# Kernel tuning notes

Hardware: AMD Instinct MI355X
Metric: run time of the kernel (lower is better)

Reference implementation:

```python
import jax, jax.numpy as jnp
import numpy as np

B = 2; QD = 128; H = QD; W = QD; NQ = QD * QD
EMBED = 256; HEADS = 8; POINTS = 4; D = EMBED // HEADS; FFN = 512


def setup_inputs() -> dict:
    key = jax.random.key(0)
    ks = jax.random.split(key, 16)
    s = 0.02
    rn = lambda k, shp: jax.random.normal(k, shp, jnp.float32) * s
    return {
        'q': jax.random.normal(ks[0], (B, NQ, EMBED), jnp.float32),
        'W_off': rn(ks[1], (EMBED, HEADS * POINTS * 2)),
        'b_off': rn(ks[2], (HEADS * POINTS * 2,)),
        'W_attn': rn(ks[3], (EMBED, HEADS * POINTS)),
        'b_attn': rn(ks[4], (HEADS * POINTS,)),
        'W_val': rn(ks[5], (EMBED, EMBED)),
        'b_val': rn(ks[6], (EMBED,)),
        'W_out': rn(ks[7], (EMBED, EMBED)),
        'b_out': rn(ks[8], (EMBED,)),
        'W1': rn(ks[9], (EMBED, FFN)),
        'b1': rn(ks[10], (FFN,)),
        'W2': rn(ks[11], (FFN, EMBED)),
        'b2': rn(ks[12], (EMBED,)),
        'gamma': jnp.ones((EMBED,), jnp.float32),
        'beta': jnp.zeros((EMBED,), jnp.float32),
    }


def _layernorm(x, g, b):
    m = x.mean(-1, keepdims=True)
    v = ((x - m) ** 2).mean(-1, keepdims=True)
    return (x - m) * jax.lax.rsqrt(v + 1e-5) * g + b


def _msda(q, W_off, b_off, W_attn, b_attn, W_val, b_val, W_out, b_out):
    # value projection; value == query here. (B, NQ, EMBED)
    value = q @ W_val + b_val
    v = value.reshape(B, NQ, HEADS, D).transpose(0, 2, 1, 3)  # (B, heads, Nv, D)

    off = (q @ W_off + b_off).reshape(B, NQ, HEADS, POINTS, 2)
    aw = jax.nn.softmax((q @ W_attn + b_attn).reshape(B, NQ, HEADS, POINTS), axis=-1)

    # reference points: torch.meshgrid(linspace, linspace, indexing='xy')
    lin = jnp.linspace(0.0, 1.0, QD)
    gx, gy = jnp.meshgrid(lin, lin, indexing='xy')
    ref = jnp.stack([gx, gy], -1).reshape(1, NQ, 1, 1, 2)

    # offset_normalizer = [W, H]; sampling locations in [0,1]
    loc = ref + off / jnp.array([W, H], jnp.float32)
    # grid_sample bilinear, align_corners=False: pixel = loc * size - 0.5
    px = (loc[..., 0] * W - 0.5).transpose(0, 2, 1, 3)  # (B, heads, NQ, P)
    py = (loc[..., 1] * H - 0.5).transpose(0, 2, 1, 3)

    x0 = jnp.floor(px)
    y0 = jnp.floor(py)
    sampled = jnp.zeros((B, HEADS, NQ, POINTS, D), jnp.float32)
    for dy in (0.0, 1.0):
        for dx in (0.0, 1.0):
            xi = x0 + dx
            yi = y0 + dy
            wgt = (1.0 - jnp.abs(px - xi)) * (1.0 - jnp.abs(py - yi))
            valid = ((xi >= 0) & (xi <= W - 1) & (yi >= 0) & (yi <= H - 1)).astype(jnp.float32)
            idx = (jnp.clip(yi, 0, H - 1).astype(jnp.int32) * W
                   + jnp.clip(xi, 0, W - 1).astype(jnp.int32))  # (B, heads, NQ, P)
            g = jnp.take_along_axis(v, idx.reshape(B, HEADS, NQ * POINTS, 1), axis=2)
            g = g.reshape(B, HEADS, NQ, POINTS, D)
            sampled = sampled + g * (wgt * valid)[..., None]

    awt = aw.transpose(0, 2, 1, 3)  # (B, heads, NQ, P)
    out = (sampled * awt[..., None]).sum(3)  # (B, heads, NQ, D)
    out = out.transpose(0, 2, 1, 3).reshape(B, NQ, EMBED)
    # mmcv: dropout(output_proj(out)) + identity ; dropout is identity at eval
    return out @ W_out + b_out + q


def reference(q, W_off, b_off, W_attn, b_attn, W_val, b_val, W_out, b_out,
              W1, b1, W2, b2, gamma, beta):
    attn = _msda(q, W_off, b_off, W_attn, b_attn, W_val, b_val, W_out, b_out)
    x = attn + q  # outer residual in the module (in addition to mmcv's internal one)
    ffn = _layernorm(jax.nn.relu(x @ W1 + b1) @ W2 + b2, gamma, beta)
    return x + ffn
```

## Files before the change

### kernel.cpp

```cpp
#include <hip/hip_runtime.h>
#include <hip/hip_bf16.h>
#include <cstddef>
#include <cstdint>

#define B_      2
#define QD_     128
#define NQ_     (QD_ * QD_)
#define EMBED_  256
#define HEADS_  8
#define POINTS_ 4
#define FFN_    512
#define RTOT_   (B_ * NQ_)
#define NCATP_  384

using bf16x8 = __attribute__((ext_vector_type(8))) short;
using f32x4  = __attribute__((ext_vector_type(4))) float;

__device__ __forceinline__ short f2bf(float f) {
    unsigned u = __float_as_uint(f);
    u += 0x7FFFu + ((u >> 16) & 1u);
    return (short)(u >> 16);
}
__device__ __forceinline__ float bf2f(short s) {
    return __uint_as_float(((unsigned)(unsigned short)s) << 16);
}

#define GLDS(gp, lp) __builtin_amdgcn_global_load_lds( \
        (const __attribute__((address_space(1))) void*)(gp), \
        (__attribute__((address_space(3))) void*)(lp), 16, 0, 0)

#define WCAT_ELEMS  (NCATP_ * 256)
#define WOUT_ELEMS  (256 * 256)
#define W1_ELEMS    (512 * 256)
#define W2_ELEMS    (256 * 512)
#define PREP_TOTAL  (WCAT_ELEMS + WOUT_ELEMS + W1_ELEMS + W2_ELEMS)
#define CVT_BLOCKS  (RTOT_ * EMBED_ / 8 / 256)
#define PREP_BLOCKS ((PREP_TOTAL + 255) / 256)

__global__ __launch_bounds__(256) void prep_all(
        const float* __restrict__ q, short* __restrict__ qbf,
        const float* __restrict__ Wv, const float* __restrict__ Wo,
        const float* __restrict__ Wa, const float* __restrict__ bv,
        const float* __restrict__ bo, const float* __restrict__ ba,
        const float* __restrict__ W_out, const float* __restrict__ W1,
        const float* __restrict__ W2,
        short* __restrict__ WcatT, short* __restrict__ WoutT,
        short* __restrict__ W1T, short* __restrict__ W2T,
        float* __restrict__ bcat) {
    const int b = blockIdx.x;
    if (b < CVT_BLOCKS) {
        const size_t i = (size_t)b * 256 + threadIdx.x;
        const float4 f0 = *(const float4*)(q + i * 8);
        const float4 f1 = *(const float4*)(q + i * 8 + 4);
        bf16x8 v;
        v[0] = f2bf(f0.x); v[1] = f2bf(f0.y); v[2] = f2bf(f0.z); v[3] = f2bf(f0.w);
        v[4] = f2bf(f1.x); v[5] = f2bf(f1.y); v[6] = f2bf(f1.z); v[7] = f2bf(f1.w);
        *(bf16x8*)(qbf + i * 8) = v;
        return;
    }
    int idx = (b - CVT_BLOCKS) * 256 + threadIdx.x;
    if (idx < WCAT_ELEMS) {
        int c = idx >> 8, k = idx & 255;
        float v = 0.f;
        if (c < 256)      v = Wv[k * 256 + c];
        else if (c < 320) v = Wo[k * 64 + (c - 256)];
        else if (c < 352) v = Wa[k * 32 + (c - 320)];
        WcatT[idx] = f2bf(v);
    } else if (idx < WCAT_ELEMS + WOUT_ELEMS) {
        int j = idx - WCAT_ELEMS; int c = j >> 8, k = j & 255;
        WoutT[j] = f2bf(W_out[k * 256 + c]);
    } else if (idx < WCAT_ELEMS + WOUT_ELEMS + W1_ELEMS) {
        int j = idx - (WCAT_ELEMS + WOUT_ELEMS); int c = j >> 8, k = j & 255;
        W1T[j] = f2bf(W1[k * 512 + c]);
    } else if (idx < PREP_TOTAL) {
        int j = idx - (WCAT_ELEMS + WOUT_ELEMS + W1_ELEMS); int c = j >> 9, k = j & 511;
        W2T[j] = f2bf(W2[k * 256 + c]);
    }
    if (idx < NCATP_) {
        float v = 0.f;
        if (idx < 256)      v = bv[idx];
        else if (idx < 320) v = bo[idx - 256];
        else if (idx < 352) v = ba[idx - 320];
        bcat[idx] = v;
    }
}

enum { EP_RELU_BF16 = 1, EP_ADD2Q_BF16 = 2, EP_SPLIT = 3 };

template <int EP>
__global__ __launch_bounds__(256) void gemm_mfma(
        const short* __restrict__ A,
        const short* __restrict__ Bt,
        const float* __restrict__ bias,
        const short* __restrict__ extra,
        float* __restrict__ Cf,
        short* __restrict__ Cb,
        int M, int N, int K) {
    __shared__ __align__(16) short As[2][128 * 64];
    __shared__ __align__(16) short Bs[2][128 * 64];

    const int t    = threadIdx.x;
    const int ln   = t & 63;
    const int w    = t >> 6;
    const int wr   = w >> 1;
    const int wc   = w & 1;
    const int lrow = ln & 15;
    const int lkg  = ln >> 4;

    const int gx   = gridDim.x;
    const int nwg  = gx * gridDim.y;
    const int flat = blockIdx.y * gx + blockIdx.x;
    const int q8   = nwg >> 3;
    const int swz  = (flat & 7) * q8 + (flat >> 3);
    const int row0 = (swz / gx) * 128;
    const int col0 = (swz % gx) * 128;

    f32x4 acc[4][4] = {};

    auto stage = [&](int buf, int k0) {
        #pragma unroll
        for (int j = 0; j < 4; ++j) {
            const int c0 = (w * 4 + j) * 64;
            const int c  = c0 + ln;
            const int r  = c >> 3;
            const int s  = (c & 7) ^ (r & 7);
            GLDS(A  + (size_t)(row0 + r) * K + (k0 + s * 8), &As[buf][c0 * 8]);
            GLDS(Bt + (size_t)(col0 + r) * K + (k0 + s * 8), &Bs[buf][c0 * 8]);
        }
    };

    stage(0, 0);
    __syncthreads();
    int cur = 0;
    for (int k0 = 0; k0 < K; k0 += 64) {
        if (k0 + 64 < K) stage(cur ^ 1, k0 + 64);
        #pragma unroll
        for (int ks = 0; ks < 2; ++ks) {
            const int slot = ((ks * 4 + lkg) ^ (lrow & 7)) * 8;
            bf16x8 af[4], bfr[4];
            #pragma unroll
            for (int m = 0; m < 4; ++m)
                af[m] = *(const bf16x8*)&As[cur][(wr * 64 + m * 16 + lrow) * 64 + slot];
            #pragma unroll
            for (int n = 0; n < 4; ++n)
                bfr[n] = *(const bf16x8*)&Bs[cur][(wc * 64 + n * 16 + lrow) * 64 + slot];
            #pragma unroll
            for (int m = 0; m < 4; ++m)
                #pragma unroll
                for (int n = 0; n < 4; ++n)
                    acc[m][n] = __builtin_amdgcn_mfma_f32_16x16x32_bf16(
                        af[m], bfr[n], acc[m][n], 0, 0, 0);
        }
        __syncthreads();
        cur ^= 1;
    }

    const int orow = (ln >> 4) * 4;
    const int ocol = ln & 15;
    #pragma unroll
    for (int m = 0; m < 4; ++m) {
        #pragma unroll
        for (int n = 0; n < 4; ++n) {
            const int col = col0 + wc * 64 + n * 16 + ocol;
            const float bv = bias[col];
            #pragma unroll
            for (int rr = 0; rr < 4; ++rr) {
                const int row = row0 + wr * 64 + m * 16 + orow + rr;
                float v = acc[m][n][rr] + bv;
                if (EP == EP_SPLIT) {
                    if (col < 256) Cb[(size_t)row * 256 + col] = f2bf(v);
                    else           Cf[(size_t)row * 128 + (col - 256)] = v;
                } else if (EP == EP_RELU_BF16) {
                    Cb[(size_t)row * N + col] = f2bf(fmaxf(v, 0.f));
                } else if (EP == EP_ADD2Q_BF16) {
                    v += 2.f * bf2f(extra[(size_t)row * N + col]);
                    Cb[(size_t)row * N + col] = f2bf(v);
                }
            }
        }
    }
}

__global__ __launch_bounds__(256) void gemm_ln(
        const short* __restrict__ A,
        const short* __restrict__ Bt,
        const float* __restrict__ bias,
        const short* __restrict__ xres,
        const float* __restrict__ gamma, const float* __restrict__ beta,
        float* __restrict__ out, int M, int K) {
    __shared__ __align__(16) short As[2][64 * 64];
    __shared__ __align__(16) short Bs[256 * 64];
    __shared__ float red[64][4][2];

    const int t    = threadIdx.x;
    const int ln   = t & 63;
    const int w    = t >> 6;
    const int lrow = ln & 15;
    const int lkg  = ln >> 4;
    const int row0 = blockIdx.x * 64;

    f32x4 acc[4][4] = {};

    auto stage_a = [&](int buf, int k0) {
        #pragma unroll
        for (int j = 0; j < 2; ++j) {
            const int c0 = (w * 2 + j) * 64;
            const int c  = c0 + ln;
            const int r  = c >> 3;
            const int s  = (c & 7) ^ (r & 7);
            GLDS(A + (size_t)(row0 + r) * K + (k0 + s * 8), &As[buf][c0 * 8]);
        }
    };
    auto stage_b = [&](int k0) {
        #pragma unroll
        for (int j = 0; j < 8; ++j) {
            const int c0 = (w * 8 + j) * 64;
            const int c  = c0 + ln;
            const int r  = c >> 3;
            const int s  = (c & 7) ^ (r & 7);
            GLDS(Bt + (size_t)r * K + (k0 + s * 8), &Bs[c0 * 8]);
        }
    };

    stage_a(0, 0);
    stage_b(0);
    __syncthreads();
    int buf = 0;
    for (int kt = 0; kt < 8; ++kt) {
        if (kt < 7) stage_a(buf ^ 1, kt * 64 + 64);
        #pragma unroll
        for (int ks = 0; ks < 2; ++ks) {
            const int slot = ((ks * 4 + lkg) ^ (lrow & 7)) * 8;
            bf16x8 af[4], bfr[4];
            #pragma unroll
            for (int m = 0; m < 4; ++m)
                af[m] = *(const bf16x8*)&As[buf][(m * 16 + lrow) * 64 + slot];
            #pragma unroll
            for (int n = 0; n < 4; ++n)
                bfr[n] = *(const bf16x8*)&Bs[(w * 64 + n * 16 + lrow) * 64 + slot];
            #pragma unroll
            for (int m = 0; m < 4; ++m)
                #pragma unroll
                for (int n = 0; n < 4; ++n)
                    acc[m][n] = __builtin_amdgcn_mfma_f32_16x16x32_bf16(
                        af[m], bfr[n], acc[m][n], 0, 0, 0);
        }
        __syncthreads();
        if (kt < 7) {
            stage_b(kt * 64 + 64);
            __syncthreads();
        }
        buf ^= 1;
    }

    const int orow = lkg * 4;
    const int ocol = lrow;

    #pragma unroll
    for (int n = 0; n < 4; ++n) {
        const float bv = bias[w * 64 + n * 16 + ocol];
        #pragma unroll
        for (int m = 0; m < 4; ++m)
            #pragma unroll
            for (int rr = 0; rr < 4; ++rr)
                acc[m][n][rr] += bv;
    }

    #pragma unroll
    for (int m = 0; m < 4; ++m) {
        #pragma unroll
        for (int rr = 0; rr < 4; ++rr) {
            float s = 0.f, sq = 0.f;
            #pragma unroll
            for (int n = 0; n < 4; ++n) {
                const float v = acc[m][n][rr];
                s += v; sq += v * v;
            }
            #pragma unroll
            for (int o = 1; o < 16; o <<= 1) {
                s  += __shfl_xor(s, o, 64);
                sq += __shfl_xor(sq, o, 64);
            }
            if (ocol == 0) {
                const int row = m * 16 + orow + rr;
                red[row][w][0] = s;
                red[row][w][1] = sq;
            }
        }
    }
    __syncthreads();

    #pragma unroll
    for (int m = 0; m < 4; ++m) {
        #pragma unroll
        for (int rr = 0; rr < 4; ++rr) {
            const int row = m * 16 + orow + rr;
            const float S  = red[row][0][0] + red[row][1][0] + red[row][2][0] + red[row][3][0];
            const float SQ = red[row][0][1] + red[row][1][1] + red[row][2][1] + red[row][3][1];
            const float mean = S * (1.0f / 256.0f);
            const float var  = SQ * (1.0f / 256.0f) - mean * mean;
            const float rs   = rsqrtf(var + 1e-5f);
            const size_t rbase = (size_t)(row0 + row) * 256;
            #pragma unroll
            for (int n = 0; n < 4; ++n) {
                const int col = w * 64 + n * 16 + ocol;
                out[rbase + col] = bf2f(xres[rbase + col])
                                 + (acc[m][n][rr] - mean) * rs * gamma[col] + beta[col];
            }
        }
    }
}

__global__ __launch_bounds__(256) void msda_sample(
        const float* __restrict__ pm, const short* __restrict__ vcomp,
        short* __restrict__ msda) {
    __shared__ int   s_off[8][32][4];
    __shared__ float s_c[8][32][4];

    const int t  = threadIdx.x;
    const int r0 = blockIdx.x * 8;
    const int bq = r0 >> 14;

    {
        const int g = t >> 5, cmb = t & 31, h = cmb >> 2, p = cmb & 3;
        const int r = r0 + g;
        const int n = r & (NQ_ - 1);
        const int gi = n >> 7, gj = n & 127;
        const float* pr = pm + (size_t)r * 128;

        const float l0 = pr[64 + h * 4 + 0], l1 = pr[64 + h * 4 + 1];
        const float l2 = pr[64 + h * 4 + 2], l3 = pr[64 + h * 4 + 3];
        const float mx = fmaxf(fmaxf(l0, l1), fmaxf(l2, l3));
        const float sum = expf(l0 - mx) + expf(l1 - mx) + expf(l2 - mx) + expf(l3 - mx);
        const float lp = pr[64 + h * 4 + p];
        const float aw = expf(lp - mx) / sum;

        const float ox = pr[h * 8 + p * 2 + 0];
        const float oy = pr[h * 8 + p * 2 + 1];
        const float px = (gj * (1.0f / 127.0f) + ox * (1.0f / 128.0f)) * 128.0f - 0.5f;
        const float py = (gi * (1.0f / 127.0f) + oy * (1.0f / 128.0f)) * 128.0f - 0.5f;
        const float x0f = floorf(px), y0f = floorf(py);
        const int   x0 = (int)x0f, y0 = (int)y0f;
        const float fx = px - x0f, fy = py - y0f;
        const int x0c = min(max(x0, 0), 127), x1c = min(max(x0 + 1, 0), 127);
        const int y0c = min(max(y0, 0), 127), y1c = min(max(y0 + 1, 0), 127);
        const float vx0 = ((unsigned)x0 <= 127u) ? 1.f : 0.f;
        const float vx1 = ((unsigned)(x0 + 1) <= 127u) ? 1.f : 0.f;
        const float vy0 = ((unsigned)y0 <= 127u) ? 1.f : 0.f;
        const float vy1 = ((unsigned)(y0 + 1) <= 127u) ? 1.f : 0.f;

        s_off[g][cmb][0] = (y0c * 128 + x0c) * 512;
        s_off[g][cmb][1] = (y0c * 128 + x1c) * 512;
        s_off[g][cmb][2] = (y1c * 128 + x0c) * 512;
        s_off[g][cmb][3] = (y1c * 128 + x1c) * 512;
        s_c[g][cmb][0] = aw * (1.f - fx) * (1.f - fy) * vx0 * vy0;
        s_c[g][cmb][1] = aw * fx * (1.f - fy) * vx1 * vy0;
        s_c[g][cmb][2] = aw * (1.f - fx) * fy * vx0 * vy1;
        s_c[g][cmb][3] = aw * fx * fy * vx1 * vy1;
    }
    __syncthreads();

    const int half = t >> 7;
    const int h    = (t >> 4) & 7;
    const int dd   = t & 15;
    const char* vb = (const char*)vcomp + ((size_t)bq * NQ_ * 256 + h * 32 + dd * 2) * 2;

    #pragma unroll
    for (int it = 0; it < 4; ++it) {
        const int g = it * 2 + half;
        float a0 = 0.f, a1 = 0.f;
        #pragma unroll
        for (int p = 0; p < 4; ++p) {
            const int cmb = h * 4 + p;
            #pragma unroll
            for (int k = 0; k < 4; ++k) {
                const unsigned u = *(const unsigned*)(vb + s_off[g][cmb][k]);
                const float c = s_c[g][cmb][k];
                a0 += c * __uint_as_float(u << 16);
                a1 += c * __uint_as_float(u & 0xffff0000u);
            }
        }
        const int r = r0 + g;
        const unsigned o = (unsigned)(unsigned short)f2bf(a0)
                         | ((unsigned)(unsigned short)f2bf(a1) << 16);
        *(unsigned*)&msda[(size_t)r * 256 + h * 32 + dd * 2] = o;
    }
}

extern "C" void kernel_launch(void* const* d_in, const int* in_sizes, int n_in,
                              void* d_out, int out_size, void* d_ws, size_t ws_size,
                              hipStream_t stream) {
    const float* q      = (const float*)d_in[0];
    const float* b_out  = (const float*)d_in[8];
    const float* b1     = (const float*)d_in[10];
    const float* b2     = (const float*)d_in[12];
    const float* gamma  = (const float*)d_in[13];
    const float* beta   = (const float*)d_in[14];

    float* out = (float*)d_out;

    char* w = (char*)d_ws;
    float* pm    = (float*)w; w += (size_t)RTOT_ * 128 * 4;
    short* vcomp = (short*)w; w += (size_t)RTOT_ * 256 * 2;
    short* qbf   = (short*)w; w += (size_t)RTOT_ * EMBED_ * 2;
    short* msda  = (short*)w; w += (size_t)RTOT_ * EMBED_ * 2;
    short* xbf   = (short*)w; w += (size_t)RTOT_ * EMBED_ * 2;
    short* hid   = (short*)w; w += (size_t)RTOT_ * FFN_ * 2;
    short* WcatT = (short*)w; w += WCAT_ELEMS * 2;
    short* WoutT = (short*)w; w += WOUT_ELEMS * 2;
    short* W1T   = (short*)w; w += W1_ELEMS * 2;
    short* W2T   = (short*)w; w += W2_ELEMS * 2;
    float* bcat  = (float*)w; w += NCATP_ * 4;

    prep_all<<<CVT_BLOCKS + PREP_BLOCKS, 256, 0, stream>>>(
        q, qbf,
        (const float*)d_in[5], (const float*)d_in[1], (const float*)d_in[3],
        (const float*)d_in[6], (const float*)d_in[2], (const float*)d_in[4],
        (const float*)d_in[7], (const float*)d_in[9], (const float*)d_in[11],
        WcatT, WoutT, W1T, W2T, bcat);

    gemm_mfma<EP_SPLIT><<<dim3(NCATP_ / 128, RTOT_ / 128), 256, 0, stream>>>(
        qbf, WcatT, bcat, nullptr, pm, vcomp, RTOT_, NCATP_, EMBED_);

    msda_sample<<<RTOT_ / 8, 256, 0, stream>>>(pm, vcomp, msda);

    gemm_mfma<EP_ADD2Q_BF16><<<dim3(EMBED_ / 128, RTOT_ / 128), 256, 0, stream>>>(
        msda, WoutT, b_out, qbf, nullptr, xbf, RTOT_, EMBED_, EMBED_);

    gemm_mfma<EP_RELU_BF16><<<dim3(FFN_ / 128, RTOT_ / 128), 256, 0, stream>>>(
        xbf, W1T, b1, nullptr, nullptr, hid, RTOT_, FFN_, EMBED_);

    gemm_ln<<<RTOT_ / 64, 256, 0, stream>>>(
        hid, W2T, b2, xbf, gamma, beta, out, RTOT_, FFN_);
}
```

Baseline: 105.9 us.

## Fuse output projection and FFN first layer into one kernel

Replaces the separate W_out GEMM (with residual) and the W1 GEMM (with ReLU) by one 512-thread kernel per 128-row tile. It keeps the x tile in shared memory and feeds it straight into the FFN1 GEMM, so x is not re-read from global memory and one launch is removed. The cost is fewer workgroups (256 instead of 512 and 1024), single-buffered loads without double buffering, and about 112KB of LDS per block, which lowers occupancy.

Result: faster. 103.3 us (-2.5%).

```diff
diff --git a/kernel.cpp b/kernel.cpp
--- a/kernel.cpp
+++ b/kernel.cpp
@@ -85,14 +85,13 @@
     }
 }
 
-enum { EP_RELU_BF16 = 1, EP_ADD2Q_BF16 = 2, EP_SPLIT = 3 };
+enum { EP_SPLIT = 3 };
 
 template <int EP>
 __global__ __launch_bounds__(256) void gemm_mfma(
         const short* __restrict__ A,
         const short* __restrict__ Bt,
         const float* __restrict__ bias,
-        const short* __restrict__ extra,
         float* __restrict__ Cf,
         short* __restrict__ Cb,
         int M, int N, int K) {
@@ -167,14 +166,140 @@
             for (int rr = 0; rr < 4; ++rr) {
                 const int row = row0 + wr * 64 + m * 16 + orow + rr;
                 float v = acc[m][n][rr] + bv;
-                if (EP == EP_SPLIT) {
-                    if (col < 256) Cb[(size_t)row * 256 + col] = f2bf(v);
-                    else           Cf[(size_t)row * 128 + (col - 256)] = v;
-                } else if (EP == EP_RELU_BF16) {
-                    Cb[(size_t)row * N + col] = f2bf(fmaxf(v, 0.f));
-                } else if (EP == EP_ADD2Q_BF16) {
-                    v += 2.f * bf2f(extra[(size_t)row * N + col]);
-                    Cb[(size_t)row * N + col] = f2bf(v);
+                if (col < 256) Cb[(size_t)row * 256 + col] = f2bf(v);
+                else           Cf[(size_t)row * 128 + (col - 256)] = v;
+            }
+        }
+    }
+}
+
+__global__ __launch_bounds__(512) void gemm_x_ffn1(
+        const short* __restrict__ msda,
+        const short* __restrict__ WoutT,
+        const float* __restrict__ b_out,
+        const short* __restrict__ qbf,
+        const short* __restrict__ W1T,
+        const float* __restrict__ b1,
+        short* __restrict__ xbf,
+        short* __restrict__ hid) {
+    __shared__ __align__(16) short xs[128 * 256];
+    __shared__ __align__(16) short stg[128 * 192];
+    short* As = stg;
+    short* Bs = stg + 128 * 64;
+
+    const int t    = threadIdx.x;
+    const int ln   = t & 63;
+    const int w    = t >> 6;
+    const int wr   = w >> 2;
+    const int wc   = w & 3;
+    const int lrow = ln & 15;
+    const int lkg  = ln >> 4;
+    const int row0 = blockIdx.x * 128;
+    const int orow = lkg * 4;
+    const int ocol = lrow;
+
+    f32x4 acc[4][4] = {};
+    for (int kt = 0; kt < 4; ++kt) {
+        #pragma unroll
+        for (int j = 0; j < 2; ++j) {
+            const int c0 = (w * 2 + j) * 64;
+            const int cc = c0 + ln;
+            const int r  = cc >> 3;
+            const int s  = (cc & 7) ^ (r & 7);
+            GLDS(msda + (size_t)(row0 + r) * 256 + kt * 64 + s * 8, &As[c0 * 8]);
+        }
+        #pragma unroll
+        for (int j = 0; j < 4; ++j) {
+            const int c0 = (w * 4 + j) * 64;
+            const int cc = c0 + ln;
+            const int r  = cc >> 3;
+            const int s  = (cc & 7) ^ (r & 7);
+            GLDS(WoutT + (size_t)r * 256 + kt * 64 + s * 8, &Bs[c0 * 8]);
+        }
+        __syncthreads();
+        #pragma unroll
+        for (int ks = 0; ks < 2; ++ks) {
+            const int slot = ((ks * 4 + lkg) ^ (lrow & 7)) * 8;
+            bf16x8 af[4], bfr[4];
+            #pragma unroll
+            for (int m = 0; m < 4; ++m)
+                af[m] = *(const bf16x8*)&As[(wr * 64 + m * 16 + lrow) * 64 + slot];
+            #pragma unroll
+            for (int n = 0; n < 4; ++n)
+                bfr[n] = *(const bf16x8*)&Bs[(wc * 64 + n * 16 + lrow) * 64 + slot];
+            #pragma unroll
+            for (int m = 0; m < 4; ++m)
+                #pragma unroll
+                for (int n = 0; n < 4; ++n)
+                    acc[m][n] = __builtin_amdgcn_mfma_f32_16x16x32_bf16(
+                        af[m], bfr[n], acc[m][n], 0, 0, 0);
+        }
+        __syncthreads();
+    }
+
+    #pragma unroll
+    for (int m = 0; m < 4; ++m) {
+        #pragma unroll
+        for (int n = 0; n < 4; ++n) {
+            const int kk  = n * 16 + ocol;
+            const int col = wc * 64 + kk;
+            const float bv = b_out[col];
+            #pragma unroll
+            for (int rr = 0; rr < 4; ++rr) {
+                const int row = wr * 64 + m * 16 + orow + rr;
+                float v = acc[m][n][rr] + bv
+                        + 2.f * bf2f(qbf[(size_t)(row0 + row) * 256 + col]);
+                const short bb = f2bf(v);
+                xbf[(size_t)(row0 + row) * 256 + col] = bb;
+                xs[wc * 8192 + row * 64 + ((kk >> 3) ^ (row & 7)) * 8 + (kk & 7)] = bb;
+            }
+        }
+    }
+    __syncthreads();
+
+    #pragma unroll 1
+    for (int p = 0; p < 2; ++p) {
+        f32x4 acc2[4][4] = {};
+        for (int kt = 0; kt < 4; ++kt) {
+            #pragma unroll
+            for (int j = 0; j < 4; ++j) {
+                const int c0 = (w * 4 + j) * 64;
+                const int cc = c0 + ln;
+                const int r  = cc >> 3;
+                const int s  = (cc & 7) ^ (r & 7);
+                GLDS(W1T + (size_t)(p * 256 + r) * 256 + kt * 64 + s * 8, &Bs[c0 * 8]);
+            }
+            __syncthreads();
+            #pragma unroll
+            for (int ks = 0; ks < 2; ++ks) {
+                const int slot = ((ks * 4 + lkg) ^ (lrow & 7)) * 8;
+                bf16x8 af[4], bfr[4];
+                #pragma unroll
+                for (int m = 0; m < 4; ++m)
+                    af[m] = *(const bf16x8*)&xs[kt * 8192 + (wr * 64 + m * 16 + lrow) * 64 + slot];
+                #pragma unroll
+                for (int n = 0; n < 4; ++n)
+                    bfr[n] = *(const bf16x8*)&Bs[(wc * 64 + n * 16 + lrow) * 64 + slot];
+                #pragma unroll
+                for (int m = 0; m < 4; ++m)
+                    #pragma unroll
+                    for (int n = 0; n < 4; ++n)
+                        acc2[m][n] = __builtin_amdgcn_mfma_f32_16x16x32_bf16(
+                            af[m], bfr[n], acc2[m][n], 0, 0, 0);
+            }
+            __syncthreads();
+        }
+        #pragma unroll
+        for (int m = 0; m < 4; ++m) {
+            #pragma unroll
+            for (int n = 0; n < 4; ++n) {
+                const int col = p * 256 + wc * 64 + n * 16 + ocol;
+                const float bv = b1[col];
+                #pragma unroll
+                for (int rr = 0; rr < 4; ++rr) {
+                    const int row = wr * 64 + m * 16 + orow + rr;
+                    hid[(size_t)(row0 + row) * 512 + col] =
+                        f2bf(fmaxf(acc2[m][n][rr] + bv, 0.f));
                 }
             }
         }
@@ -420,15 +545,12 @@
         WcatT, WoutT, W1T, W2T, bcat);
 
     gemm_mfma<EP_SPLIT><<<dim3(NCATP_ / 128, RTOT_ / 128), 256, 0, stream>>>(
-        qbf, WcatT, bcat, nullptr, pm, vcomp, RTOT_, NCATP_, EMBED_);
+        qbf, WcatT, bcat, pm, vcomp, RTOT_, NCATP_, EMBED_);
 
     msda_sample<<<RTOT_ / 8, 256, 0, stream>>>(pm, vcomp, msda);
 
-    gemm_mfma<EP_ADD2Q_BF16><<<dim3(EMBED_ / 128, RTOT_ / 128), 256, 0, stream>>>(
-        msda, WoutT, b_out, qbf, nullptr, xbf, RTOT_, EMBED_, EMBED_);
-
-    gemm_mfma<EP_RELU_BF16><<<dim3(FFN_ / 128, RTOT_ / 128), 256, 0, stream>>>(
-        xbf, W1T, b1, nullptr, nullptr, hid, RTOT_, FFN_, EMBED_);
+    gemm_x_ffn1<<<RTOT_ / 128, 512, 0, stream>>>(
+        msda, WoutT, b_out, qbf, W1T, b1, xbf, hid);
 
     gemm_ln<<<RTOT_ / 64, 256, 0, stream>>>(
         hid, W2T, b2, xbf, gamma, beta, out, RTOT_, FFN_);
```
